# Performance work log

Hardware: AMD Instinct MI355X
Metric: run time of the kernel (lower is better)

## Reference

```python
import jax, jax.numpy as jnp
import numpy as np

N_NODES = 50000
C = 256          # in_channels == hidden_size
E = 800000


def setup_inputs() -> dict:
    key = jax.random.key(0)
    ks = jax.random.split(key, 12)
    x = jax.random.normal(ks[0], (N_NODES, C), dtype=jnp.float32)
    edge_index = jax.random.randint(ks[1], (2, E), 0, N_NODES, dtype=jnp.int64)
    edge_attr = jax.random.uniform(ks[2], (E,), dtype=jnp.float32)
    edge_weights_index = jax.random.randint(ks[3], (2, E), 0, N_NODES, dtype=jnp.int64)
    s = 1.0 / np.sqrt(C)
    # TopKPooling projection vector
    p_pool = jax.random.normal(ks[4], (C,), dtype=jnp.float32) * s
    # GRU (input=C, hidden=C): gates stacked [r, z, n]
    W_ih = jax.random.normal(ks[5], (3 * C, C), dtype=jnp.float32) * s
    W_hh = jax.random.normal(ks[6], (3 * C, C), dtype=jnp.float32) * s
    b_ih = jnp.zeros((3 * C,), dtype=jnp.float32)
    b_hh = jnp.zeros((3 * C,), dtype=jnp.float32)
    # initial evolving GCN weight [C, C]
    W_init = jax.random.normal(ks[7], (C, C), dtype=jnp.float32) * s
    # EdgeDecoder MLP
    lin1_w = jax.random.normal(ks[8], (C, 2 * C), dtype=jnp.float32) / np.sqrt(2 * C)
    lin1_b = jnp.zeros((C,), dtype=jnp.float32)
    lin2_w = jax.random.normal(ks[9], (1, C), dtype=jnp.float32) * s
    lin2_b = jnp.zeros((1,), dtype=jnp.float32)
    return {
        "x": x, "edge_index": edge_index, "edge_attr": edge_attr,
        "edge_weights_index": edge_weights_index,
        "p_pool": p_pool, "W_ih": W_ih, "W_hh": W_hh, "b_ih": b_ih, "b_hh": b_hh,
        "W_init": W_init, "lin1_w": lin1_w, "lin1_b": lin1_b,
        "lin2_w": lin2_w, "lin2_b": lin2_b,
    }


def _forward(x, edge_attr, p_pool, W_ih, W_hh, b_ih, b_hh, W_init,
             lin1_w, lin1_b, lin2_w, lin2_b, edge_index, edge_weights_index):
    n_nodes, c = x.shape
    # --- EvolveGCNH: TopK pooling summary (k = in_channels) ---
    score = x @ p_pool / jnp.linalg.norm(p_pool)          # [N]
    top_score, perm = jax.lax.top_k(score, c)             # [C]
    x_tilde = x[perm] * jnp.tanh(top_score)[:, None]      # [C, C]
    # --- GRU step: input x_tilde (batch=C), hidden = evolving weight W_init ---
    gi = x_tilde @ W_ih.T + b_ih                           # [C, 3C]
    gh = W_init @ W_hh.T + b_hh                            # [C, 3C]
    i_r, i_z, i_n = jnp.split(gi, 3, axis=1)
    h_r, h_z, h_n = jnp.split(gh, 3, axis=1)
    r = jax.nn.sigmoid(i_r + h_r)
    z = jax.nn.sigmoid(i_z + h_z)
    n = jnp.tanh(i_n + r * h_n)
    W = (1.0 - z) * n + z * W_init                         # [C, C] evolved GCN weight
    # --- GCNConv with fixed W, add_self_loops=False ---
    xw = x @ W                                             # [N, C]
    src, dst = edge_index[0], edge_index[1]
    deg = jax.ops.segment_sum(edge_attr, dst, num_segments=n_nodes)
    dinv = jnp.where(deg > 0, jax.lax.rsqrt(jnp.where(deg > 0, deg, 1.0)), 0.0)
    norm = dinv[src] * edge_attr * dinv[dst]               # [E]
    node_emb = jax.ops.segment_sum(xw[src] * norm[:, None], dst,
                                   num_segments=n_nodes)   # [N, C]
    # --- EdgeDecoder: gather src/trg, concat, MLP ---
    s_idx, t_idx = edge_weights_index[0], edge_weights_index[1]
    edge_emb = jnp.concatenate([node_emb[s_idx], node_emb[t_idx]], axis=1)  # [E, 2C]
    h = jax.nn.relu(edge_emb @ lin1_w.T + lin1_b)          # [E, C]
    pred = h @ lin2_w.T + lin2_b                           # [E, 1]
    return pred.reshape(-1)


def reference(x, edge_index, edge_attr, edge_weights_index, p_pool,
              W_ih, W_hh, b_ih, b_hh, W_init, lin1_w, lin1_b, lin2_w, lin2_b):
    # dropout is identity in eval mode
    return _forward(x, edge_attr, p_pool, W_ih, W_hh, b_ih, b_hh, W_init,
                    lin1_w, lin1_b, lin2_w, lin2_b, edge_index, edge_weights_index)
```

## Files before the change

### kernel.cpp

```cpp
#include <hip/hip_runtime.h>
#include <hip/hip_bf16.h>
#include <math.h>


typedef __attribute__((ext_vector_type(8))) short bf16x8;
typedef __attribute__((ext_vector_type(8))) unsigned short u16x8;
typedef __attribute__((ext_vector_type(4))) float f32x4;

#define WSHIFT 9
#define WMASK 511
#define NBUCK 98

__device__ __forceinline__ unsigned f2key(float f) {
  unsigned u = __float_as_uint(f);
  return (u & 0x80000000u) ? ~u : (u | 0x80000000u);
}

__device__ __forceinline__ unsigned short f2bf(float f) {
  unsigned u = __float_as_uint(f);
  unsigned r = u + 0x7fffu + ((u >> 16) & 1u);
  return (unsigned short)(r >> 16);
}
__device__ __forceinline__ float bf2f(unsigned short h) {
  return __uint_as_float((unsigned)h << 16);
}

template <int CTRL>
__device__ __forceinline__ float dpp_add(float s) {
  int t = __builtin_amdgcn_update_dpp(0, __float_as_int(s), CTRL, 0xf, 0xf, false);
  return s + __int_as_float(t);
}

__device__ __forceinline__ void gload16(const void* g, void* l) {
  __builtin_amdgcn_global_load_lds((const __attribute__((address_space(1))) void*)g,
                                   (__attribute__((address_space(3))) void*)l, 16, 0, 0);
}

__global__ __launch_bounds__(256) void init_kernel(const float* __restrict__ lin1,
                                                   unsigned short* __restrict__ WAB,
                                                   int4* __restrict__ zb, int nz4) {
  int b = blockIdx.x, tid = threadIdx.x;
  if (b < 512) {
    int idx = b * 256 + tid;
    int n = idx >> 9, k = idx & 511;
    unsigned short h = f2bf(lin1[idx]);
    if (k < 256)
      WAB[n * 256 + k] = h;
    else
      WAB[(256 + n) * 256 + (k - 256)] = h;
  } else {
    int j = (b - 512) * 256 + tid;
    if (j < nz4) zb[j] = make_int4(0, 0, 0, 0);
  }
}

__global__ __launch_bounds__(256) void score_cast_kernel(const float* __restrict__ x,
                                                         const float* __restrict__ p,
                                                         float* __restrict__ score,
                                                         unsigned short* __restrict__ xh, int N) {
  int node = blockIdx.x * 4 + (threadIdx.x >> 6);
  int lane = threadIdx.x & 63;
  if (node >= N) return;
  float4 xv = ((const float4*)(x + (size_t)node * 256))[lane];
  ushort4 hv;
  hv.x = f2bf(xv.x);
  hv.y = f2bf(xv.y);
  hv.z = f2bf(xv.z);
  hv.w = f2bf(xv.w);
  ((ushort4*)(xh + (size_t)node * 256))[lane] = hv;
  float4 pv = ((const float4*)p)[lane];
  float s = xv.x * pv.x + xv.y * pv.y + xv.z * pv.z + xv.w * pv.w;
  float sp = pv.x * pv.x + pv.y * pv.y + pv.z * pv.z + pv.w * pv.w;
#pragma unroll
  for (int off = 32; off > 0; off >>= 1) {
    s += __shfl_down(s, off, 64);
    sp += __shfl_down(sp, off, 64);
  }
  if (lane == 0) score[node] = s / sqrtf(sp);
}

__global__ __launch_bounds__(256) void hist12_kernel(const float* __restrict__ score, int n,
                                                     int* __restrict__ gh) {
  __shared__ int lh[4096];
  int tid = threadIdx.x;
  for (int i = tid; i < 4096; i += 256) lh[i] = 0;
  __syncthreads();
  int idx = blockIdx.x * 256 + tid;
  int stride = gridDim.x * 256;
  for (int i = idx; i < n; i += stride) {
    unsigned key = f2key(score[i]);
    atomicAdd(&lh[key >> 20], 1);
  }
  __syncthreads();
  for (int i = tid; i < 4096; i += 256) {
    int v = lh[i];
    if (v) atomicAdd(&gh[i], v);
  }
}

__global__ __launch_bounds__(1024) void topk_kernel(const float* __restrict__ score, int n, int k,
                                                    const int* __restrict__ gh,
                                                    int* __restrict__ perm,
                                                    float* __restrict__ tts) {
  __shared__ int part[1024];
  __shared__ unsigned sT;
  int tid = threadIdx.x;
  {
    int b0 = tid * 4;
    int s0 = gh[b0], s1 = gh[b0 + 1], s2 = gh[b0 + 2], s3 = gh[b0 + 3];
    part[tid] = s0 + s1 + s2 + s3;
    __syncthreads();
    for (int off = 1; off < 1024; off <<= 1) {
      int v = part[tid];
      int add = (tid + off < 1024) ? part[tid + off] : 0;
      __syncthreads();
      part[tid] = v + add;
      __syncthreads();
    }
    int sufChunk = part[tid];
    int sufNext = (tid < 1023) ? part[tid + 1] : 0;
    if (sufNext < k && sufChunk >= k) {
      int run = sufNext;
      int b;
      run += s3;
      if (run >= k) b = b0 + 3;
      else {
        run += s2;
        if (run >= k) b = b0 + 2;
        else {
          run += s1;
          b = (run >= k) ? b0 + 1 : b0;
        }
      }
      sT = ((unsigned)b) << 20;
    }
  }
  __syncthreads();
  unsigned T = sT;
  __shared__ unsigned keys[1024];
  __shared__ int idxs[1024];
  __shared__ int cnt;
  if (tid == 0) cnt = 0;
  keys[tid] = 0u;
  idxs[tid] = 0x7fffffff;
  __syncthreads();
  for (int i = tid; i < n; i += 1024) {
    unsigned key = f2key(score[i]);
    if (key >= T) {
      int p = atomicAdd(&cnt, 1);
      if (p < 1024) { keys[p] = key; idxs[p] = i; }
    }
  }
  __syncthreads();
  for (int size = 2; size <= 1024; size <<= 1) {
    for (int stride = size >> 1; stride > 0; stride >>= 1) {
      int j = tid ^ stride;
      if (j > tid) {
        unsigned ka = keys[tid], kb = keys[j];
        int ia = idxs[tid], ib = idxs[j];
        bool aBefore = (ka > kb) || (ka == kb && ia < ib);
        bool up = ((tid & size) == 0);
        if (aBefore != up) {
          keys[tid] = kb; keys[j] = ka;
          idxs[tid] = ib; idxs[j] = ia;
        }
      }
      __syncthreads();
    }
  }
  if (tid < k) {
    int idx = idxs[tid];
    perm[tid] = idx;
    tts[tid] = tanhf(score[idx]);
  }
}

__global__ __launch_bounds__(256) void gru_kernel(const float* __restrict__ x,
                                                  const int* __restrict__ perm,
                                                  const float* __restrict__ tts,
                                                  const float* __restrict__ Wi,
                                                  const float* __restrict__ W_ih,
                                                  const float* __restrict__ W_hh,
                                                  const float* __restrict__ b_ih,
                                                  const float* __restrict__ b_hh,
                                                  unsigned short* __restrict__ WevoT) {
  int i = blockIdx.x, j = threadIdx.x;
  __shared__ float sx[256], sh[256];
  sx[j] = x[(size_t)perm[i] * 256 + j] * tts[i];
  sh[j] = Wi[i * 256 + j];
  __syncthreads();
  float gi[3], gh[3];
#pragma unroll
  for (int g = 0; g < 3; ++g) {
    int row = g * 256 + j;
    const float4* wi4 = (const float4*)(W_ih + (size_t)row * 256);
    const float4* wh4 = (const float4*)(W_hh + (size_t)row * 256);
    float si = 0.f, s2 = 0.f;
    for (int k4 = 0; k4 < 64; ++k4) {
      float4 wv = wi4[k4];
      float4 hv = wh4[k4];
      int k = k4 * 4;
      si += sx[k] * wv.x + sx[k + 1] * wv.y + sx[k + 2] * wv.z + sx[k + 3] * wv.w;
      s2 += sh[k] * hv.x + sh[k + 1] * hv.y + sh[k + 2] * hv.z + sh[k + 3] * hv.w;
    }
    gi[g] = si + b_ih[row];
    gh[g] = s2 + b_hh[row];
  }
  float r = 1.f / (1.f + expf(-(gi[0] + gh[0])));
  float z = 1.f / (1.f + expf(-(gi[1] + gh[1])));
  float nn = tanhf(gi[2] + r * gh[2]);
  float w = (1.f - z) * nn + z * sh[j];
  WevoT[(size_t)j * 256 + i] = f2bf(w);
}

__global__ __launch_bounds__(512) void mfma_gemm128(const unsigned short* __restrict__ A,
                                                    const unsigned short* __restrict__ BT,
                                                    unsigned short* __restrict__ C1,
                                                    unsigned short* __restrict__ C2,
                                                    int M) {
  __shared__ unsigned short sA[128 * 32];
  __shared__ unsigned short sB[256 * 32];
  int tid = threadIdx.x;
  int wave = tid >> 6, lane = tid & 63;
  int quad = lane >> 4, r16 = lane & 15;
  int wm = wave >> 2, wn = wave & 3;
  int mbase = blockIdx.x * 128;
  const unsigned short* Bt = BT + ((size_t)blockIdx.y << 16);
  unsigned short* Cout = blockIdx.y ? C2 : C1;

  int srow = tid >> 2, scolq = tid & 3;
  const unsigned short* gA = A + (size_t)(mbase + srow) * 256 + scolq * 8;
  const unsigned short* gB0 = Bt + (size_t)srow * 256 + scolq * 8;
  const unsigned short* gB1 = Bt + (size_t)(128 + srow) * 256 + scolq * 8;
  unsigned short* lA = sA + wave * 512;
  unsigned short* lB0 = sB + wave * 512;
  unsigned short* lB1 = sB + 4096 + wave * 512;

  f32x4 acc[4][4];
#pragma unroll
  for (int i = 0; i < 4; ++i)
#pragma unroll
    for (int j = 0; j < 4; ++j) acc[i][j] = (f32x4){0.f, 0.f, 0.f, 0.f};

  const unsigned short* pA = sA + (wm * 64 + r16) * 32 + quad * 8;
  const unsigned short* pB = sB + (wn * 64 + r16) * 32 + quad * 8;

  for (int k0 = 0; k0 < 256; k0 += 32) {
    if (k0) __syncthreads();
    gload16(gA + k0, lA);
    gload16(gB0 + k0, lB0);
    gload16(gB1 + k0, lB1);
    __syncthreads();
    bf16x8 af[4], bfr[4];
#pragma unroll
    for (int mt = 0; mt < 4; ++mt) af[mt] = *(const bf16x8*)(pA + mt * 512);
#pragma unroll
    for (int nt = 0; nt < 4; ++nt) bfr[nt] = *(const bf16x8*)(pB + nt * 512);
#pragma unroll
    for (int mt = 0; mt < 4; ++mt)
#pragma unroll
      for (int nt = 0; nt < 4; ++nt)
        acc[mt][nt] = __builtin_amdgcn_mfma_f32_16x16x32_bf16(af[mt], bfr[nt], acc[mt][nt], 0, 0, 0);
  }
#pragma unroll
  for (int mt = 0; mt < 4; ++mt) {
#pragma unroll
    for (int rr = 0; rr < 4; ++rr) {
      int grow = mbase + wm * 64 + mt * 16 + quad * 4 + rr;
      if (grow < M) {
#pragma unroll
        for (int nt = 0; nt < 4; ++nt)
          Cout[(size_t)grow * 256 + wn * 64 + nt * 16 + r16] = f2bf(acc[mt][nt][rr]);
      }
    }
  }
}


__global__ __launch_bounds__(256) void bucket_hist_kernel(const int* __restrict__ ei,
                                                          const int* __restrict__ ewi,
                                                          int* __restrict__ bcnt1,
                                                          int* __restrict__ bcnt2, int E) {
  __shared__ int c1[128], c2[128];
  int tid = threadIdx.x;
  if (tid < 128) { c1[tid] = 0; c2[tid] = 0; }
  __syncthreads();
  int idx = blockIdx.x * 256 + tid;
  int stride = gridDim.x * 256;
  for (int e = idx; e < E; e += stride) {
    atomicAdd(&c1[ei[E + e] >> WSHIFT], 1);
    atomicAdd(&c2[ewi[e] >> WSHIFT], 1);
  }
  __syncthreads();
  if (tid < 128) {
    if (c1[tid]) atomicAdd(&bcnt1[tid], c1[tid]);
    if (c2[tid]) atomicAdd(&bcnt2[tid], c2[tid]);
  }
}

__global__ __launch_bounds__(128) void bucket_scan_kernel(const int* __restrict__ bcnt1,
                                                          const int* __restrict__ bcnt2,
                                                          int* __restrict__ bbase1,
                                                          int* __restrict__ bbase2,
                                                          int* __restrict__ gcur1,
                                                          int* __restrict__ gcur2,
                                                          int* __restrict__ rowp1,
                                                          int* __restrict__ rowp2, int N, int E) {
  __shared__ int ss[128];
  int tid = threadIdx.x;
  int v = (tid < NBUCK) ? bcnt1[tid] : 0;
  ss[tid] = v;
  __syncthreads();
  for (int off = 1; off < 128; off <<= 1) {
    int a = ss[tid];
    int b = (tid >= off) ? ss[tid - off] : 0;
    __syncthreads();
    ss[tid] = a + b;
    __syncthreads();
  }
  int excl = ss[tid] - v;
  if (tid < NBUCK) { bbase1[tid] = excl; gcur1[tid] = excl; }
  if (tid == NBUCK - 1) bbase1[NBUCK] = excl + v;
  __syncthreads();
  v = (tid < NBUCK) ? bcnt2[tid] : 0;
  ss[tid] = v;
  __syncthreads();
  for (int off = 1; off < 128; off <<= 1) {
    int a = ss[tid];
    int b = (tid >= off) ? ss[tid - off] : 0;
    __syncthreads();
    ss[tid] = a + b;
    __syncthreads();
  }
  excl = ss[tid] - v;
  if (tid < NBUCK) { bbase2[tid] = excl; gcur2[tid] = excl; }
  if (tid == NBUCK - 1) bbase2[NBUCK] = excl + v;
  if (tid == 0) { rowp1[N] = E; rowp2[N] = E; }
}

__global__ __launch_bounds__(256) void p1_both_kernel(const int* __restrict__ ei,
                                                      const float* __restrict__ attr,
                                                      int* __restrict__ gcur1,
                                                      int2* __restrict__ stage1,
                                                      const int* __restrict__ ewi,
                                                      int* __restrict__ gcur2,
                                                      int2* __restrict__ stage2,
                                                      int E, int nb) {
  __shared__ int cnt[128], cur[128];
  int tid = threadIdx.x;
  bool conv = blockIdx.x < nb;
  int base = (conv ? blockIdx.x : blockIdx.x - nb) * 4096;
  int* gcur = conv ? gcur1 : gcur2;
  int2* stage = conv ? stage1 : stage2;
  if (tid < 128) cnt[tid] = 0;
  __syncthreads();
  int bk[16];
  int2 pl[16];
#pragma unroll
  for (int i = 0; i < 16; ++i) {
    int e = base + i * 256 + tid;
    bk[i] = -1;
    if (e < E) {
      if (conv) {
        int d = ei[E + e];
        int s = ei[e];
        bk[i] = d >> WSHIFT;
        pl[i] = make_int2(s | ((d & WMASK) << 16), __float_as_int(attr[e]));
      } else {
        int s = ewi[e];
        int d = ewi[E + e];
        bk[i] = s >> WSHIFT;
        pl[i] = make_int2(d | ((s & WMASK) << 16), e);
      }
      atomicAdd(&cnt[bk[i]], 1);
    }
  }
  __syncthreads();
  if (tid < NBUCK) {
    int c = cnt[tid];
    cur[tid] = c ? atomicAdd(&gcur[tid], c) : 0;
  }
  __syncthreads();
#pragma unroll
  for (int i = 0; i < 16; ++i) {
    if (bk[i] >= 0) {
      int pos = atomicAdd(&cur[bk[i]], 1);
      stage[pos] = pl[i];
    }
  }
}

__global__ __launch_bounds__(256) void p2_kernel(const int2* __restrict__ stage1,
                                                 const int* __restrict__ bbase1,
                                                 int2* __restrict__ esv,
                                                 int* __restrict__ rowp1,
                                                 float* __restrict__ dinv,
                                                 const int2* __restrict__ stage2,
                                                 const int* __restrict__ bbase2,
                                                 int2* __restrict__ eto,
                                                 int* __restrict__ rowp2, int N) {
  __shared__ int cnt[512];
  __shared__ float degs[512];
  __shared__ int pref[512];
  __shared__ int ss[256];
  int tid = threadIdx.x;
  bool isConv = blockIdx.x < NBUCK;
  int b = isConv ? blockIdx.x : blockIdx.x - NBUCK;
  const int2* stage = isConv ? stage1 : stage2;
  const int* bbase = isConv ? bbase1 : bbase2;
  int beg = bbase[b], end = bbase[b + 1];
  int node0 = b << WSHIFT;
  cnt[tid] = 0; cnt[tid + 256] = 0;
  degs[tid] = 0.f; degs[tid + 256] = 0.f;
  __syncthreads();
  for (int j = beg + tid; j < end; j += 256) {
    int2 p = stage[j];
    int loc = p.x >> 16;
    atomicAdd(&cnt[loc], 1);
    if (isConv) atomicAdd(&degs[loc], __int_as_float(p.y));
  }
  __syncthreads();
  int c0 = cnt[2 * tid], c1 = cnt[2 * tid + 1];
  ss[tid] = c0 + c1;
  __syncthreads();
  for (int off = 1; off < 256; off <<= 1) {
    int a = ss[tid];
    int bb = (tid >= off) ? ss[tid - off] : 0;
    __syncthreads();
    ss[tid] = a + bb;
    __syncthreads();
  }
  int excl = (tid ? ss[tid - 1] : 0);
  pref[2 * tid] = excl;
  pref[2 * tid + 1] = excl + c0;
  __syncthreads();
#pragma unroll
  for (int h = 0; h < 2; ++h) {
    int i = tid + h * 256;
    int node = node0 + i;
    if (node < N) {
      if (isConv) {
        rowp1[node] = beg + pref[i];
        float d = degs[i];
        dinv[node] = d > 0.f ? 1.f / sqrtf(d) : 0.f;
      } else {
        rowp2[node] = beg + pref[i];
      }
    }
  }
  __syncthreads();
  int2* outb = isConv ? esv : eto;
  for (int j = beg + tid; j < end; j += 256) {
    int2 p = stage[j];
    int loc = p.x >> 16;
    int pos = beg + atomicAdd(&pref[loc], 1);
    outb[pos] = make_int2(p.x & 0xFFFF, p.y);
  }
}

__global__ __launch_bounds__(256) void gcn_gather(const unsigned short* __restrict__ xw,
                                                  const int* __restrict__ row_ptr,
                                                  const int2* __restrict__ esv,
                                                  const float* __restrict__ dinv,
                                                  unsigned short* __restrict__ ne, int N) {
  int node = blockIdx.x * 4 + (threadIdx.x >> 6);
  int lane = threadIdx.x & 63;
  int g = lane & 15, q = lane >> 4;
  if (node >= N) return;
  int beg = row_ptr[node], end = row_ptr[node + 1];
  float acc[16];
#pragma unroll
  for (int c = 0; c < 16; ++c) acc[c] = 0.f;
  const unsigned short* xb = xw + g * 16;

  for (int cb = beg; cb < end; cb += 64) {
    int cend = cb + 64 < end ? cb + 64 : end;
    int me = cb + lane;
    int2 mm = (me < cend) ? esv[me] : make_int2(0, 0);
    int mx = mm.x;
    float mv = __int_as_float(mm.y) * dinv[mx];

    float vA = 0.f, vB = 0.f, vC = 0.f;
    u16x8 rAa, rAb, rBa, rBb, rCa, rCb;
    {
      int e = cb + q;
      int sx = __shfl(mx, q, 64);
      float tv = __shfl(mv, q, 64);
      vA = (e < cend) ? tv : 0.f;
      rAa = *(const u16x8*)(xb + (size_t)sx * 256);
      rAb = *(const u16x8*)(xb + (size_t)sx * 256 + 8);
    }
    if (cb + 4 < cend) {
      int e = cb + 4 + q;
      int sx = __shfl(mx, 4 + q, 64);
      float tv = __shfl(mv, 4 + q, 64);
      vB = (e < cend) ? tv : 0.f;
      rBa = *(const u16x8*)(xb + (size_t)sx * 256);
      rBb = *(const u16x8*)(xb + (size_t)sx * 256 + 8);
    } else { rBa = rAa; rBb = rAb; }
    if (cb + 8 < cend) {
      int e = cb + 8 + q;
      int sx = __shfl(mx, 8 + q, 64);
      float tv = __shfl(mv, 8 + q, 64);
      vC = (e < cend) ? tv : 0.f;
      rCa = *(const u16x8*)(xb + (size_t)sx * 256);
      rCb = *(const u16x8*)(xb + (size_t)sx * 256 + 8);
    } else { rCa = rAa; rCb = rAb; }

    for (int jb = cb; jb < cend; jb += 12) {
#pragma unroll
      for (int c = 0; c < 8; ++c) acc[c] += bf2f(rAa[c]) * vA;
#pragma unroll
      for (int c = 0; c < 8; ++c) acc[8 + c] += bf2f(rAb[c]) * vA;
      vA = 0.f;
      if (jb + 12 < cend) {
        int e = jb + 12 + q;
        int idx = (e - cb) & 63;
        int sx = __shfl(mx, idx, 64);
        float tv = __shfl(mv, idx, 64);
        vA = (e < cend) ? tv : 0.f;
        rAa = *(const u16x8*)(xb + (size_t)sx * 256);
        rAb = *(const u16x8*)(xb + (size_t)sx * 256 + 8);
      }
#pragma unroll
      for (int c = 0; c < 8; ++c) acc[c] += bf2f(rBa[c]) * vB;
#pragma unroll
      for (int c = 0; c < 8; ++c) acc[8 + c] += bf2f(rBb[c]) * vB;
      vB = 0.f;
      if (jb + 16 < cend) {
        int e = jb + 16 + q;
        int idx = (e - cb) & 63;
        int sx = __shfl(mx, idx, 64);
        float tv = __shfl(mv, idx, 64);
        vB = (e < cend) ? tv : 0.f;
        rBa = *(const u16x8*)(xb + (size_t)sx * 256);
        rBb = *(const u16x8*)(xb + (size_t)sx * 256 + 8);
      }
#pragma unroll
      for (int c = 0; c < 8; ++c) acc[c] += bf2f(rCa[c]) * vC;
#pragma unroll
      for (int c = 0; c < 8; ++c) acc[8 + c] += bf2f(rCb[c]) * vC;
      vC = 0.f;
      if (jb + 20 < cend) {
        int e = jb + 20 + q;
        int idx = (e - cb) & 63;
        int sx = __shfl(mx, idx, 64);
        float tv = __shfl(mv, idx, 64);
        vC = (e < cend) ? tv : 0.f;
        rCa = *(const u16x8*)(xb + (size_t)sx * 256);
        rCb = *(const u16x8*)(xb + (size_t)sx * 256 + 8);
      }
    }
  }
#pragma unroll
  for (int c = 0; c < 16; ++c) {
    acc[c] += __shfl_xor(acc[c], 16, 64);
    acc[c] += __shfl_xor(acc[c], 32, 64);
  }
  if (q == 0) {
    float dd = dinv[node];
    u16x8 o0, o1;
#pragma unroll
    for (int c = 0; c < 8; ++c) {
      o0[c] = f2bf(acc[c] * dd);
      o1[c] = f2bf(acc[8 + c] * dd);
    }
    *(u16x8*)(ne + (size_t)node * 256 + g * 16) = o0;
    *(u16x8*)(ne + (size_t)node * 256 + g * 16 + 8) = o1;
  }
}

__global__ __launch_bounds__(256) void edge_decode_csr(const unsigned short* __restrict__ A,
                                                       const unsigned short* __restrict__ Bm,
                                                       const int* __restrict__ row_ptr,
                                                       const int2* __restrict__ eto,
                                                       const float* __restrict__ b1,
                                                       const float* __restrict__ w2,
                                                       const float* __restrict__ b2,
                                                       float* __restrict__ out, int N) {
  int node = blockIdx.x * 4 + (threadIdx.x >> 6);
  int lane = threadIdx.x & 63;
  int g = lane & 15, q = lane >> 4;
  if (node >= N) return;
  int beg = row_ptr[node], end = row_ptr[node + 1];
  if (beg >= end) return;
  float a[16], w[16];
  {
    u16x8 a0 = *(const u16x8*)(A + (size_t)node * 256 + g * 16);
    u16x8 a1 = *(const u16x8*)(A + (size_t)node * 256 + g * 16 + 8);
    const float4* bp = (const float4*)(b1 + g * 16);
    const float4* wp = (const float4*)(w2 + g * 16);
#pragma unroll
    for (int i = 0; i < 4; ++i) {
      float4 bv = bp[i];
      float4 wv = wp[i];
      a[i * 4 + 0] = (i < 2 ? bf2f(a0[i * 4 + 0]) : bf2f(a1[i * 4 - 8])) + bv.x;
      a[i * 4 + 1] = (i < 2 ? bf2f(a0[i * 4 + 1]) : bf2f(a1[i * 4 - 7])) + bv.y;
      a[i * 4 + 2] = (i < 2 ? bf2f(a0[i * 4 + 2]) : bf2f(a1[i * 4 - 6])) + bv.z;
      a[i * 4 + 3] = (i < 2 ? bf2f(a0[i * 4 + 3]) : bf2f(a1[i * 4 - 5])) + bv.w;
      w[i * 4 + 0] = wv.x;
      w[i * 4 + 1] = wv.y;
      w[i * 4 + 2] = wv.z;
      w[i * 4 + 3] = wv.w;
    }
  }
  float base = b2[0];
  const unsigned short* Bb = Bm + g * 16;

  for (int cb = beg; cb < end; cb += 64) {
    int cend = cb + 64 < end ? cb + 64 : end;
    int me = cb + lane;
    int2 mm = (me < cend) ? eto[me] : make_int2(0, 0);
    int mx = mm.x, my = mm.y;

    bool okA = false, okB = false, okC = false;
    int oA = 0, oB = 0, oC = 0;
    u16x8 rAa, rAb, rBa, rBb, rCa, rCb;
    {
      int e = cb + q;
      int sx = __shfl(mx, q, 64);
      oA = __shfl(my, q, 64);
      okA = e < cend;
      rAa = *(const u16x8*)(Bb + (size_t)sx * 256);
      rAb = *(const u16x8*)(Bb + (size_t)sx * 256 + 8);
    }
    if (cb + 4 < cend) {
      int e = cb + 4 + q;
      int sx = __shfl(mx, 4 + q, 64);
      oB = __shfl(my, 4 + q, 64);
      okB = e < cend;
      rBa = *(const u16x8*)(Bb + (size_t)sx * 256);
      rBb = *(const u16x8*)(Bb + (size_t)sx * 256 + 8);
    } else { rBa = rAa; rBb = rAb; }
    if (cb + 8 < cend) {
      int e = cb + 8 + q;
      int sx = __shfl(mx, 8 + q, 64);
      oC = __shfl(my, 8 + q, 64);
      okC = e < cend;
      rCa = *(const u16x8*)(Bb + (size_t)sx * 256);
      rCb = *(const u16x8*)(Bb + (size_t)sx * 256 + 8);
    } else { rCa = rAa; rCb = rAb; }

    for (int jb = cb; jb < cend; jb += 12) {
      {
        float s0 = 0.f, s1 = 0.f;
#pragma unroll
        for (int c = 0; c < 8; ++c) s0 += fmaxf(a[c] + bf2f(rAa[c]), 0.f) * w[c];
#pragma unroll
        for (int c = 0; c < 8; ++c) s1 += fmaxf(a[8 + c] + bf2f(rAb[c]), 0.f) * w[8 + c];
        float s = s0 + s1;
        s = dpp_add<0x128>(s);
        s = dpp_add<0x124>(s);
        s = dpp_add<0x122>(s);
        s = dpp_add<0x121>(s);
        if (g == 0 && okA) out[oA] = s + base;
      }
      okA = false;
      if (jb + 12 < cend) {
        int e = jb + 12 + q;
        int idx = (e - cb) & 63;
        int sx = __shfl(mx, idx, 64);
        oA = __shfl(my, idx, 64);
        okA = e < cend;
        rAa = *(const u16x8*)(Bb + (size_t)sx * 256);
        rAb = *(const u16x8*)(Bb + (size_t)sx * 256 + 8);
      }
      {
        float s0 = 0.f, s1 = 0.f;
#pragma unroll
        for (int c = 0; c < 8; ++c) s0 += fmaxf(a[c] + bf2f(rBa[c]), 0.f) * w[c];
#pragma unroll
        for (int c = 0; c < 8; ++c) s1 += fmaxf(a[8 + c] + bf2f(rBb[c]), 0.f) * w[8 + c];
        float s = s0 + s1;
        s = dpp_add<0x128>(s);
        s = dpp_add<0x124>(s);
        s = dpp_add<0x122>(s);
        s = dpp_add<0x121>(s);
        if (g == 0 && okB) out[oB] = s + base;
      }
      okB = false;
      if (jb + 16 < cend) {
        int e = jb + 16 + q;
        int idx = (e - cb) & 63;
        int sx = __shfl(mx, idx, 64);
        oB = __shfl(my, idx, 64);
        okB = e < cend;
        rBa = *(const u16x8*)(Bb + (size_t)sx * 256);
        rBb = *(const u16x8*)(Bb + (size_t)sx * 256 + 8);
      }
      {
        float s0 = 0.f, s1 = 0.f;
#pragma unroll
        for (int c = 0; c < 8; ++c) s0 += fmaxf(a[c] + bf2f(rCa[c]), 0.f) * w[c];
#pragma unroll
        for (int c = 0; c < 8; ++c) s1 += fmaxf(a[8 + c] + bf2f(rCb[c]), 0.f) * w[8 + c];
        float s = s0 + s1;
        s = dpp_add<0x128>(s);
        s = dpp_add<0x124>(s);
        s = dpp_add<0x122>(s);
        s = dpp_add<0x121>(s);
        if (g == 0 && okC) out[oC] = s + base;
      }
      okC = false;
      if (jb + 20 < cend) {
        int e = jb + 20 + q;
        int idx = (e - cb) & 63;
        int sx = __shfl(mx, idx, 64);
        oC = __shfl(my, idx, 64);
        okC = e < cend;
        rCa = *(const u16x8*)(Bb + (size_t)sx * 256);
        rCb = *(const u16x8*)(Bb + (size_t)sx * 256 + 8);
      }
    }
  }
}

extern "C" void kernel_launch(void* const* d_in, const int* in_sizes, int n_in,
                              void* d_out, int out_size, void* d_ws, size_t ws_size,
                              hipStream_t stream) {
  const float* x      = (const float*)d_in[0];
  const int*   ei     = (const int*)d_in[1];
  const float* attr   = (const float*)d_in[2];
  const int*   ewi    = (const int*)d_in[3];
  const float* p_pool = (const float*)d_in[4];
  const float* W_ih   = (const float*)d_in[5];
  const float* W_hh   = (const float*)d_in[6];
  const float* b_ih   = (const float*)d_in[7];
  const float* b_hh   = (const float*)d_in[8];
  const float* W_init = (const float*)d_in[9];
  const float* lin1_w = (const float*)d_in[10];
  const float* lin1_b = (const float*)d_in[11];
  const float* lin2_w = (const float*)d_in[12];
  const float* lin2_b = (const float*)d_in[13];
  float* out = (float*)d_out;

  const int C = 256;
  const int N = in_sizes[0] / C;
  const int E = in_sizes[2];

  char* ws = (char*)d_ws;
  size_t off = 0;
  auto alloc = [&](size_t bytes) {
    size_t o = off;
    off = (off + bytes + 255) & ~(size_t)255;
    return o;
  };
  float*          score  = (float*)(ws + alloc((size_t)N * 4));
  int*            perm   = (int*)(ws + alloc(C * 4));
  float*          tts    = (float*)(ws + alloc(C * 4));
  unsigned short* WevoT  = (unsigned short*)(ws + alloc((size_t)C * C * 2));
  unsigned short* WAB    = (unsigned short*)(ws + alloc((size_t)2 * C * C * 2));
  int   zeroInts = 4096 + 128 + 128;
  char* zbase    = ws + alloc((size_t)zeroInts * 4);
  int* ghist = (int*)zbase;
  int* bcnt1 = (int*)(zbase + 4096 * 4);
  int* bcnt2 = (int*)(zbase + 4096 * 4 + 128 * 4);
  int*            bbase1 = (int*)(ws + alloc((NBUCK + 1) * 4));
  int*            bbase2 = (int*)(ws + alloc((NBUCK + 1) * 4));
  int*            gcur1  = (int*)(ws + alloc(128 * 4));
  int*            gcur2  = (int*)(ws + alloc(128 * 4));
  float*          dinv   = (float*)(ws + alloc((size_t)N * 4));
  int*            rowp1  = (int*)(ws + alloc((size_t)(N + 1) * 4));
  int*            rowp2  = (int*)(ws + alloc((size_t)(N + 1) * 4));
  int2*           stage1 = (int2*)(ws + alloc((size_t)E * 8));
  int2*           stage2 = (int2*)(ws + alloc((size_t)E * 8));
  int2*           esv    = (int2*)(ws + alloc((size_t)E * 8));
  int2*           eto    = (int2*)(ws + alloc((size_t)E * 8));
  unsigned short* xh     = (unsigned short*)(ws + alloc((size_t)N * C * 2));
  unsigned short* xwh    = (unsigned short*)(ws + alloc((size_t)N * C * 2));
  unsigned short* Bbf    = (unsigned short*)(ws + alloc((size_t)N * C * 2));
  unsigned short* ne  = xh;
  unsigned short* Abf = xwh;

  int nz4 = (zeroInts + 3) / 4;
  int nbP1 = (E + 4095) / 4096;

  init_kernel<<<512 + (nz4 + 255) / 256, 256, 0, stream>>>(lin1_w, WAB, (int4*)zbase, nz4);

  score_cast_kernel<<<(N + 3) / 4, 256, 0, stream>>>(x, p_pool, score, xh, N);

  hist12_kernel<<<64, 256, 0, stream>>>(score, N, ghist);
  topk_kernel<<<1, 1024, 0, stream>>>(score, N, C, ghist, perm, tts);

  gru_kernel<<<C, C, 0, stream>>>(x, perm, tts, W_init, W_ih, W_hh, b_ih, b_hh, WevoT);

  mfma_gemm128<<<dim3((N + 127) / 128, 1), 512, 0, stream>>>(xh, WevoT, xwh, xwh, N);

  bucket_hist_kernel<<<256, 256, 0, stream>>>(ei, ewi, bcnt1, bcnt2, E);
  bucket_scan_kernel<<<1, 128, 0, stream>>>(bcnt1, bcnt2, bbase1, bbase2, gcur1, gcur2,
                                            rowp1, rowp2, N, E);
  p1_both_kernel<<<2 * nbP1, 256, 0, stream>>>(ei, attr, gcur1, stage1,
                                               ewi, gcur2, stage2, E, nbP1);
  p2_kernel<<<2 * NBUCK, 256, 0, stream>>>(stage1, bbase1, esv, rowp1, dinv,
                                           stage2, bbase2, eto, rowp2, N);

  gcn_gather<<<(N + 3) / 4, 256, 0, stream>>>(xwh, rowp1, esv, dinv, ne, N);

  mfma_gemm128<<<dim3((N + 127) / 128, 2), 512, 0, stream>>>(ne, WAB, Abf, Bbf, N);

  edge_decode_csr<<<(N + 3) / 4, 256, 0, stream>>>(Abf, Bbf, rowp2, eto,
                                                   lin1_b, lin2_w, lin2_b, out, N);
}
```

Baseline: 454.9 us.

## Merge independent topk/GRU and edge-bucketing stages into shared kernel launches

```diff
diff --git a/kernel.cpp b/kernel.cpp
--- a/kernel.cpp
+++ b/kernel.cpp
@@ -54,163 +54,351 @@
   }
 }
 
-__global__ __launch_bounds__(256) void score_cast_kernel(const float* __restrict__ x,
-                                                         const float* __restrict__ p,
-                                                         float* __restrict__ score,
-                                                         unsigned short* __restrict__ xh, int N) {
-  int node = blockIdx.x * 4 + (threadIdx.x >> 6);
-  int lane = threadIdx.x & 63;
-  if (node >= N) return;
-  float4 xv = ((const float4*)(x + (size_t)node * 256))[lane];
-  ushort4 hv;
-  hv.x = f2bf(xv.x);
-  hv.y = f2bf(xv.y);
-  hv.z = f2bf(xv.z);
-  hv.w = f2bf(xv.w);
-  ((ushort4*)(xh + (size_t)node * 256))[lane] = hv;
-  float4 pv = ((const float4*)p)[lane];
-  float s = xv.x * pv.x + xv.y * pv.y + xv.z * pv.z + xv.w * pv.w;
-  float sp = pv.x * pv.x + pv.y * pv.y + pv.z * pv.z + pv.w * pv.w;
-#pragma unroll
-  for (int off = 32; off > 0; off >>= 1) {
-    s += __shfl_down(s, off, 64);
-    sp += __shfl_down(sp, off, 64);
-  }
-  if (lane == 0) score[node] = s / sqrtf(sp);
-}
-
-__global__ __launch_bounds__(256) void hist12_kernel(const float* __restrict__ score, int n,
-                                                     int* __restrict__ gh) {
-  __shared__ int lh[4096];
+__global__ __launch_bounds__(256) void fusedA_kernel(const float* __restrict__ x,
+                                                     const float* __restrict__ p,
+                                                     float* __restrict__ score,
+                                                     unsigned short* __restrict__ xh, int N,
+                                                     const int* __restrict__ ei,
+                                                     const int* __restrict__ ewi,
+                                                     int* __restrict__ bcnt1,
+                                                     int* __restrict__ bcnt2, int E) {
   int tid = threadIdx.x;
-  for (int i = tid; i < 4096; i += 256) lh[i] = 0;
-  __syncthreads();
-  int idx = blockIdx.x * 256 + tid;
-  int stride = gridDim.x * 256;
-  for (int i = idx; i < n; i += stride) {
-    unsigned key = f2key(score[i]);
-    atomicAdd(&lh[key >> 20], 1);
-  }
-  __syncthreads();
-  for (int i = tid; i < 4096; i += 256) {
-    int v = lh[i];
-    if (v) atomicAdd(&gh[i], v);
-  }
-}
-
-__global__ __launch_bounds__(1024) void topk_kernel(const float* __restrict__ score, int n, int k,
-                                                    const int* __restrict__ gh,
-                                                    int* __restrict__ perm,
-                                                    float* __restrict__ tts) {
-  __shared__ int part[1024];
-  __shared__ unsigned sT;
+  if (blockIdx.x < 256) {
+    __shared__ int c1[128], c2[128];
+    if (tid < 128) { c1[tid] = 0; c2[tid] = 0; }
+    __syncthreads();
+    int idx = blockIdx.x * 256 + tid;
+    int stride = 256 * 256;
+    for (int e = idx; e < E; e += stride) {
+      atomicAdd(&c1[ei[E + e] >> WSHIFT], 1);
+      atomicAdd(&c2[ewi[e] >> WSHIFT], 1);
+    }
+    __syncthreads();
+    if (tid < 128) {
+      if (c1[tid]) atomicAdd(&bcnt1[tid], c1[tid]);
+      if (c2[tid]) atomicAdd(&bcnt2[tid], c2[tid]);
+    }
+  } else {
+    int node = (blockIdx.x - 256) * 4 + (tid >> 6);
+    int lane = tid & 63;
+    if (node >= N) return;
+    float4 xv = ((const float4*)(x + (size_t)node * 256))[lane];
+    ushort4 hv;
+    hv.x = f2bf(xv.x);
+    hv.y = f2bf(xv.y);
+    hv.z = f2bf(xv.z);
+    hv.w = f2bf(xv.w);
+    ((ushort4*)(xh + (size_t)node * 256))[lane] = hv;
+    float4 pv = ((const float4*)p)[lane];
+    float s = xv.x * pv.x + xv.y * pv.y + xv.z * pv.z + xv.w * pv.w;
+    float sp = pv.x * pv.x + pv.y * pv.y + pv.z * pv.z + pv.w * pv.w;
+#pragma unroll
+    for (int off = 32; off > 0; off >>= 1) {
+      s += __shfl_down(s, off, 64);
+      sp += __shfl_down(sp, off, 64);
+    }
+    if (lane == 0) score[node] = s / sqrtf(sp);
+  }
+}
+
+__global__ __launch_bounds__(256) void fusedB_kernel(const float* __restrict__ score, int n,
+                                                     int* __restrict__ gh,
+                                                     const int* __restrict__ bcnt1,
+                                                     const int* __restrict__ bcnt2,
+                                                     int* __restrict__ bbase1,
+                                                     int* __restrict__ bbase2,
+                                                     int* __restrict__ gcur1,
+                                                     int* __restrict__ gcur2,
+                                                     int* __restrict__ rowp1,
+                                                     int* __restrict__ rowp2, int N, int E) {
   int tid = threadIdx.x;
-  {
-    int b0 = tid * 4;
-    int s0 = gh[b0], s1 = gh[b0 + 1], s2 = gh[b0 + 2], s3 = gh[b0 + 3];
-    part[tid] = s0 + s1 + s2 + s3;
-    __syncthreads();
-    for (int off = 1; off < 1024; off <<= 1) {
-      int v = part[tid];
-      int add = (tid + off < 1024) ? part[tid + off] : 0;
+  if (blockIdx.x < 64) {
+    __shared__ int lh[4096];
+    for (int i = tid; i < 4096; i += 256) lh[i] = 0;
+    __syncthreads();
+    int idx = blockIdx.x * 256 + tid;
+    int stride = 64 * 256;
+    for (int i = idx; i < n; i += stride) {
+      unsigned key = f2key(score[i]);
+      atomicAdd(&lh[key >> 20], 1);
+    }
+    __syncthreads();
+    for (int i = tid; i < 4096; i += 256) {
+      int v = lh[i];
+      if (v) atomicAdd(&gh[i], v);
+    }
+  } else {
+    __shared__ int ss[128];
+    int v = 0;
+    if (tid < 128) { v = (tid < NBUCK) ? bcnt1[tid] : 0; ss[tid] = v; }
+    __syncthreads();
+    for (int off = 1; off < 128; off <<= 1) {
+      int a = 0, b = 0;
+      if (tid < 128) { a = ss[tid]; b = (tid >= off) ? ss[tid - off] : 0; }
       __syncthreads();
-      part[tid] = v + add;
+      if (tid < 128) ss[tid] = a + b;
       __syncthreads();
     }
-    int sufChunk = part[tid];
-    int sufNext = (tid < 1023) ? part[tid + 1] : 0;
-    if (sufNext < k && sufChunk >= k) {
-      int run = sufNext;
-      int b;
-      run += s3;
-      if (run >= k) b = b0 + 3;
-      else {
-        run += s2;
-        if (run >= k) b = b0 + 2;
+    if (tid < 128) {
+      int excl = ss[tid] - v;
+      if (tid < NBUCK) { bbase1[tid] = excl; gcur1[tid] = excl; }
+      if (tid == NBUCK - 1) bbase1[NBUCK] = excl + v;
+    }
+    __syncthreads();
+    int v2 = 0;
+    if (tid < 128) { v2 = (tid < NBUCK) ? bcnt2[tid] : 0; ss[tid] = v2; }
+    __syncthreads();
+    for (int off = 1; off < 128; off <<= 1) {
+      int a = 0, b = 0;
+      if (tid < 128) { a = ss[tid]; b = (tid >= off) ? ss[tid - off] : 0; }
+      __syncthreads();
+      if (tid < 128) ss[tid] = a + b;
+      __syncthreads();
+    }
+    if (tid < 128) {
+      int excl = ss[tid] - v2;
+      if (tid < NBUCK) { bbase2[tid] = excl; gcur2[tid] = excl; }
+      if (tid == NBUCK - 1) bbase2[NBUCK] = excl + v2;
+    }
+    if (tid == 0) { rowp1[N] = E; rowp2[N] = E; }
+  }
+}
+
+__global__ __launch_bounds__(1024) void fusedC_kernel(const int* __restrict__ ei,
+                                                      const float* __restrict__ attr,
+                                                      int* __restrict__ gcur1,
+                                                      int2* __restrict__ stage1,
+                                                      const int* __restrict__ ewi,
+                                                      int* __restrict__ gcur2,
+                                                      int2* __restrict__ stage2,
+                                                      int E, int nb,
+                                                      const float* __restrict__ score, int n, int k,
+                                                      const int* __restrict__ gh,
+                                                      int* __restrict__ perm,
+                                                      float* __restrict__ tts) {
+  int tid = threadIdx.x;
+  if ((int)blockIdx.x < 2 * nb) {
+    bool conv = (int)blockIdx.x < nb;
+    __shared__ int pcnt[128], pcur[128];
+    int base = (conv ? blockIdx.x : blockIdx.x - nb) * 8192;
+    int* gcur = conv ? gcur1 : gcur2;
+    int2* stage = conv ? stage1 : stage2;
+    if (tid < 128) pcnt[tid] = 0;
+    __syncthreads();
+    int bk[8];
+    int2 pl[8];
+#pragma unroll
+    for (int i = 0; i < 8; ++i) {
+      int e = base + i * 1024 + tid;
+      bk[i] = -1;
+      if (e < E) {
+        if (conv) {
+          int d = ei[E + e];
+          int s = ei[e];
+          bk[i] = d >> WSHIFT;
+          pl[i] = make_int2(s | ((d & WMASK) << 16), __float_as_int(attr[e]));
+        } else {
+          int s = ewi[e];
+          int d = ewi[E + e];
+          bk[i] = s >> WSHIFT;
+          pl[i] = make_int2(d | ((s & WMASK) << 16), e);
+        }
+        atomicAdd(&pcnt[bk[i]], 1);
+      }
+    }
+    __syncthreads();
+    if (tid < NBUCK) {
+      int c = pcnt[tid];
+      pcur[tid] = c ? atomicAdd(&gcur[tid], c) : 0;
+    }
+    __syncthreads();
+#pragma unroll
+    for (int i = 0; i < 8; ++i) {
+      if (bk[i] >= 0) {
+        int pos = atomicAdd(&pcur[bk[i]], 1);
+        stage[pos] = pl[i];
+      }
+    }
+  } else {
+    __shared__ int part[1024];
+    __shared__ unsigned sT;
+    {
+      int b0 = tid * 4;
+      int s0 = gh[b0], s1 = gh[b0 + 1], s2 = gh[b0 + 2], s3 = gh[b0 + 3];
+      part[tid] = s0 + s1 + s2 + s3;
+      __syncthreads();
+      for (int off = 1; off < 1024; off <<= 1) {
+        int v = part[tid];
+        int add = (tid + off < 1024) ? part[tid + off] : 0;
+        __syncthreads();
+        part[tid] = v + add;
+        __syncthreads();
+      }
+      int sufChunk = part[tid];
+      int sufNext = (tid < 1023) ? part[tid + 1] : 0;
+      if (sufNext < k && sufChunk >= k) {
+        int run = sufNext;
+        int b;
+        run += s3;
+        if (run >= k) b = b0 + 3;
         else {
-          run += s1;
-          b = (run >= k) ? b0 + 1 : b0;
+          run += s2;
+          if (run >= k) b = b0 + 2;
+          else {
+            run += s1;
+            b = (run >= k) ? b0 + 1 : b0;
+          }
         }
-      }
-      sT = ((unsigned)b) << 20;
-    }
-  }
-  __syncthreads();
-  unsigned T = sT;
-  __shared__ unsigned keys[1024];
-  __shared__ int idxs[1024];
-  __shared__ int cnt;
-  if (tid == 0) cnt = 0;
-  keys[tid] = 0u;
-  idxs[tid] = 0x7fffffff;
-  __syncthreads();
-  for (int i = tid; i < n; i += 1024) {
-    unsigned key = f2key(score[i]);
-    if (key >= T) {
-      int p = atomicAdd(&cnt, 1);
-      if (p < 1024) { keys[p] = key; idxs[p] = i; }
-    }
-  }
-  __syncthreads();
-  for (int size = 2; size <= 1024; size <<= 1) {
-    for (int stride = size >> 1; stride > 0; stride >>= 1) {
-      int j = tid ^ stride;
-      if (j > tid) {
-        unsigned ka = keys[tid], kb = keys[j];
-        int ia = idxs[tid], ib = idxs[j];
-        bool aBefore = (ka > kb) || (ka == kb && ia < ib);
-        bool up = ((tid & size) == 0);
-        if (aBefore != up) {
-          keys[tid] = kb; keys[j] = ka;
-          idxs[tid] = ib; idxs[j] = ia;
+        sT = ((unsigned)b) << 20;
+      }
+    }
+    __syncthreads();
+    unsigned T = sT;
+    __shared__ unsigned keys[1024];
+    __shared__ int idxs[1024];
+    __shared__ int cnt;
+    if (tid == 0) cnt = 0;
+    keys[tid] = 0u;
+    idxs[tid] = 0x7fffffff;
+    __syncthreads();
+    for (int i = tid; i < n; i += 1024) {
+      unsigned key = f2key(score[i]);
+      if (key >= T) {
+        int p = atomicAdd(&cnt, 1);
+        if (p < 1024) { keys[p] = key; idxs[p] = i; }
+      }
+    }
+    __syncthreads();
+    for (int size = 2; size <= 1024; size <<= 1) {
+      for (int stride = size >> 1; stride > 0; stride >>= 1) {
+        int j = tid ^ stride;
+        if (j > tid) {
+          unsigned ka = keys[tid], kb = keys[j];
+          int ia = idxs[tid], ib = idxs[j];
+          bool aBefore = (ka > kb) || (ka == kb && ia < ib);
+          bool up = ((tid & size) == 0);
+          if (aBefore != up) {
+            keys[tid] = kb; keys[j] = ka;
+            idxs[tid] = ib; idxs[j] = ia;
+          }
         }
-      }
+        __syncthreads();
+      }
+    }
+    if (tid < k) {
+      int idx = idxs[tid];
+      perm[tid] = idx;
+      tts[tid] = tanhf(score[idx]);
+    }
+  }
+}
+
+__global__ __launch_bounds__(256) void fusedD_kernel(const float* __restrict__ x,
+                                                     const int* __restrict__ perm,
+                                                     const float* __restrict__ tts,
+                                                     const float* __restrict__ Wi,
+                                                     const float* __restrict__ W_ih,
+                                                     const float* __restrict__ W_hh,
+                                                     const float* __restrict__ b_ih,
+                                                     const float* __restrict__ b_hh,
+                                                     unsigned short* __restrict__ WevoT,
+                                                     const int2* __restrict__ stage1,
+                                                     const int* __restrict__ bbase1,
+                                                     int2* __restrict__ esv,
+                                                     int* __restrict__ rowp1,
+                                                     float* __restrict__ dinv,
+                                                     const int2* __restrict__ stage2,
+                                                     const int* __restrict__ bbase2,
+                                                     int2* __restrict__ eto,
+                                                     int* __restrict__ rowp2, int N) {
+  int tid = threadIdx.x;
+  if (blockIdx.x < 256) {
+    int i = blockIdx.x, j = tid;
+    __shared__ float sx[256], sh[256];
+    sx[j] = x[(size_t)perm[i] * 256 + j] * tts[i];
+    sh[j] = Wi[i * 256 + j];
+    __syncthreads();
+    float gi[3], gh[3];
+#pragma unroll
+    for (int g = 0; g < 3; ++g) {
+      int row = g * 256 + j;
+      const float4* wi4 = (const float4*)(W_ih + (size_t)row * 256);
+      const float4* wh4 = (const float4*)(W_hh + (size_t)row * 256);
+      float si = 0.f, s2 = 0.f;
+      for (int k4 = 0; k4 < 64; ++k4) {
+        float4 wv = wi4[k4];
+        float4 hv = wh4[k4];
+        int k = k4 * 4;
+        si += sx[k] * wv.x + sx[k + 1] * wv.y + sx[k + 2] * wv.z + sx[k + 3] * wv.w;
+        s2 += sh[k] * hv.x + sh[k + 1] * hv.y + sh[k + 2] * hv.z + sh[k + 3] * hv.w;
+      }
+      gi[g] = si + b_ih[row];
+      gh[g] = s2 + b_hh[row];
+    }
+    float r = 1.f / (1.f + expf(-(gi[0] + gh[0])));
+    float z = 1.f / (1.f + expf(-(gi[1] + gh[1])));
+    float nn = tanhf(gi[2] + r * gh[2]);
+    float w = (1.f - z) * nn + z * sh[j];
+    WevoT[(size_t)j * 256 + i] = f2bf(w);
+  } else {
+    __shared__ int cnt[512];
+    __shared__ float degs[512];
+    __shared__ int pref[512];
+    __shared__ int ss[256];
+    int bb2 = blockIdx.x - 256;
+    bool isConv = bb2 < NBUCK;
+    int b = isConv ? bb2 : bb2 - NBUCK;
+    const int2* stage = isConv ? stage1 : stage2;
+    const int* bbase = isConv ? bbase1 : bbase2;
+    int beg = bbase[b], end = bbase[b + 1];
+    int node0 = b << WSHIFT;
+    cnt[tid] = 0; cnt[tid + 256] = 0;
+    degs[tid] = 0.f; degs[tid + 256] = 0.f;
+    __syncthreads();
+    for (int j = beg + tid; j < end; j += 256) {
+      int2 p = stage[j];
+      int loc = p.x >> 16;
+      atomicAdd(&cnt[loc], 1);
+      if (isConv) atomicAdd(&degs[loc], __int_as_float(p.y));
+    }
+    __syncthreads();
+    int c0 = cnt[2 * tid], c1 = cnt[2 * tid + 1];
+    ss[tid] = c0 + c1;
+    __syncthreads();
+    for (int off = 1; off < 256; off <<= 1) {
+      int a = ss[tid];
+      int bsum = (tid >= off) ? ss[tid - off] : 0;
       __syncthreads();
-    }
-  }
-  if (tid < k) {
-    int idx = idxs[tid];
-    perm[tid] = idx;
-    tts[tid] = tanhf(score[idx]);
-  }
-}
-
-__global__ __launch_bounds__(256) void gru_kernel(const float* __restrict__ x,
-                                                  const int* __restrict__ perm,
-                                                  const float* __restrict__ tts,
-                                                  const float* __restrict__ Wi,
-                                                  const float* __restrict__ W_ih,
-                                                  const float* __restrict__ W_hh,
-                                                  const float* __restrict__ b_ih,
-                                                  const float* __restrict__ b_hh,
-                                                  unsigned short* __restrict__ WevoT) {
-  int i = blockIdx.x, j = threadIdx.x;
-  __shared__ float sx[256], sh[256];
-  sx[j] = x[(size_t)perm[i] * 256 + j] * tts[i];
-  sh[j] = Wi[i * 256 + j];
-  __syncthreads();
-  float gi[3], gh[3];
-#pragma unroll
-  for (int g = 0; g < 3; ++g) {
-    int row = g * 256 + j;
-    const float4* wi4 = (const float4*)(W_ih + (size_t)row * 256);
-    const float4* wh4 = (const float4*)(W_hh + (size_t)row * 256);
-    float si = 0.f, s2 = 0.f;
-    for (int k4 = 0; k4 < 64; ++k4) {
-      float4 wv = wi4[k4];
-      float4 hv = wh4[k4];
-      int k = k4 * 4;
-      si += sx[k] * wv.x + sx[k + 1] * wv.y + sx[k + 2] * wv.z + sx[k + 3] * wv.w;
-      s2 += sh[k] * hv.x + sh[k + 1] * hv.y + sh[k + 2] * hv.z + sh[k + 3] * hv.w;
-    }
-    gi[g] = si + b_ih[row];
-    gh[g] = s2 + b_hh[row];
-  }
-  float r = 1.f / (1.f + expf(-(gi[0] + gh[0])));
-  float z = 1.f / (1.f + expf(-(gi[1] + gh[1])));
-  float nn = tanhf(gi[2] + r * gh[2]);
-  float w = (1.f - z) * nn + z * sh[j];
-  WevoT[(size_t)j * 256 + i] = f2bf(w);
+      ss[tid] = a + bsum;
+      __syncthreads();
+    }
+    int excl = (tid ? ss[tid - 1] : 0);
+    pref[2 * tid] = excl;
+    pref[2 * tid + 1] = excl + c0;
+    __syncthreads();
+#pragma unroll
+    for (int h = 0; h < 2; ++h) {
+      int i = tid + h * 256;
+      int node = node0 + i;
+      if (node < N) {
+        if (isConv) {
+          rowp1[node] = beg + pref[i];
+          float d = degs[i];
+          dinv[node] = d > 0.f ? 1.f / sqrtf(d) : 0.f;
+        } else {
+          rowp2[node] = beg + pref[i];
+        }
+      }
+    }
+    __syncthreads();
+    int2* outb = isConv ? esv : eto;
+    for (int j = beg + tid; j < end; j += 256) {
+      int2 p = stage[j];
+      int loc = p.x >> 16;
+      int pos = beg + atomicAdd(&pref[loc], 1);
+      outb[pos] = make_int2(p.x & 0xFFFF, p.y);
+    }
+  }
 }
 
 __global__ __launch_bounds__(512) void mfma_gemm128(const unsigned short* __restrict__ A,
@@ -273,188 +461,6 @@
           Cout[(size_t)grow * 256 + wn * 64 + nt * 16 + r16] = f2bf(acc[mt][nt][rr]);
       }
     }
-  }
-}
-
-
-__global__ __launch_bounds__(256) void bucket_hist_kernel(const int* __restrict__ ei,
-                                                          const int* __restrict__ ewi,
-                                                          int* __restrict__ bcnt1,
-                                                          int* __restrict__ bcnt2, int E) {
-  __shared__ int c1[128], c2[128];
-  int tid = threadIdx.x;
-  if (tid < 128) { c1[tid] = 0; c2[tid] = 0; }
-  __syncthreads();
-  int idx = blockIdx.x * 256 + tid;
-  int stride = gridDim.x * 256;
-  for (int e = idx; e < E; e += stride) {
-    atomicAdd(&c1[ei[E + e] >> WSHIFT], 1);
-    atomicAdd(&c2[ewi[e] >> WSHIFT], 1);
-  }
-  __syncthreads();
-  if (tid < 128) {
-    if (c1[tid]) atomicAdd(&bcnt1[tid], c1[tid]);
-    if (c2[tid]) atomicAdd(&bcnt2[tid], c2[tid]);
-  }
-}
-
-__global__ __launch_bounds__(128) void bucket_scan_kernel(const int* __restrict__ bcnt1,
-                                                          const int* __restrict__ bcnt2,
-                                                          int* __restrict__ bbase1,
-                                                          int* __restrict__ bbase2,
-                                                          int* __restrict__ gcur1,
-                                                          int* __restrict__ gcur2,
-                                                          int* __restrict__ rowp1,
-                                                          int* __restrict__ rowp2, int N, int E) {
-  __shared__ int ss[128];
-  int tid = threadIdx.x;
-  int v = (tid < NBUCK) ? bcnt1[tid] : 0;
-  ss[tid] = v;
-  __syncthreads();
-  for (int off = 1; off < 128; off <<= 1) {
-    int a = ss[tid];
-    int b = (tid >= off) ? ss[tid - off] : 0;
-    __syncthreads();
-    ss[tid] = a + b;
-    __syncthreads();
-  }
-  int excl = ss[tid] - v;
-  if (tid < NBUCK) { bbase1[tid] = excl; gcur1[tid] = excl; }
-  if (tid == NBUCK - 1) bbase1[NBUCK] = excl + v;
-  __syncthreads();
-  v = (tid < NBUCK) ? bcnt2[tid] : 0;
-  ss[tid] = v;
-  __syncthreads();
-  for (int off = 1; off < 128; off <<= 1) {
-    int a = ss[tid];
-    int b = (tid >= off) ? ss[tid - off] : 0;
-    __syncthreads();
-    ss[tid] = a + b;
-    __syncthreads();
-  }
-  excl = ss[tid] - v;
-  if (tid < NBUCK) { bbase2[tid] = excl; gcur2[tid] = excl; }
-  if (tid == NBUCK - 1) bbase2[NBUCK] = excl + v;
-  if (tid == 0) { rowp1[N] = E; rowp2[N] = E; }
-}
-
-__global__ __launch_bounds__(256) void p1_both_kernel(const int* __restrict__ ei,
-                                                      const float* __restrict__ attr,
-                                                      int* __restrict__ gcur1,
-                                                      int2* __restrict__ stage1,
-                                                      const int* __restrict__ ewi,
-                                                      int* __restrict__ gcur2,
-                                                      int2* __restrict__ stage2,
-                                                      int E, int nb) {
-  __shared__ int cnt[128], cur[128];
-  int tid = threadIdx.x;
-  bool conv = blockIdx.x < nb;
-  int base = (conv ? blockIdx.x : blockIdx.x - nb) * 4096;
-  int* gcur = conv ? gcur1 : gcur2;
-  int2* stage = conv ? stage1 : stage2;
-  if (tid < 128) cnt[tid] = 0;
-  __syncthreads();
-  int bk[16];
-  int2 pl[16];
-#pragma unroll
-  for (int i = 0; i < 16; ++i) {
-    int e = base + i * 256 + tid;
-    bk[i] = -1;
-    if (e < E) {
-      if (conv) {
-        int d = ei[E + e];
-        int s = ei[e];
-        bk[i] = d >> WSHIFT;
-        pl[i] = make_int2(s | ((d & WMASK) << 16), __float_as_int(attr[e]));
-      } else {
-        int s = ewi[e];
-        int d = ewi[E + e];
-        bk[i] = s >> WSHIFT;
-        pl[i] = make_int2(d | ((s & WMASK) << 16), e);
-      }
-      atomicAdd(&cnt[bk[i]], 1);
-    }
-  }
-  __syncthreads();
-  if (tid < NBUCK) {
-    int c = cnt[tid];
-    cur[tid] = c ? atomicAdd(&gcur[tid], c) : 0;
-  }
-  __syncthreads();
-#pragma unroll
-  for (int i = 0; i < 16; ++i) {
-    if (bk[i] >= 0) {
-      int pos = atomicAdd(&cur[bk[i]], 1);
-      stage[pos] = pl[i];
-    }
-  }
-}
-
-__global__ __launch_bounds__(256) void p2_kernel(const int2* __restrict__ stage1,
-                                                 const int* __restrict__ bbase1,
-                                                 int2* __restrict__ esv,
-                                                 int* __restrict__ rowp1,
-                                                 float* __restrict__ dinv,
-                                                 const int2* __restrict__ stage2,
-                                                 const int* __restrict__ bbase2,
-                                                 int2* __restrict__ eto,
-                                                 int* __restrict__ rowp2, int N) {
-  __shared__ int cnt[512];
-  __shared__ float degs[512];
-  __shared__ int pref[512];
-  __shared__ int ss[256];
-  int tid = threadIdx.x;
-  bool isConv = blockIdx.x < NBUCK;
-  int b = isConv ? blockIdx.x : blockIdx.x - NBUCK;
-  const int2* stage = isConv ? stage1 : stage2;
-  const int* bbase = isConv ? bbase1 : bbase2;
-  int beg = bbase[b], end = bbase[b + 1];
-  int node0 = b << WSHIFT;
-  cnt[tid] = 0; cnt[tid + 256] = 0;
-  degs[tid] = 0.f; degs[tid + 256] = 0.f;
-  __syncthreads();
-  for (int j = beg + tid; j < end; j += 256) {
-    int2 p = stage[j];
-    int loc = p.x >> 16;
-    atomicAdd(&cnt[loc], 1);
-    if (isConv) atomicAdd(&degs[loc], __int_as_float(p.y));
-  }
-  __syncthreads();
-  int c0 = cnt[2 * tid], c1 = cnt[2 * tid + 1];
-  ss[tid] = c0 + c1;
-  __syncthreads();
-  for (int off = 1; off < 256; off <<= 1) {
-    int a = ss[tid];
-    int bb = (tid >= off) ? ss[tid - off] : 0;
-    __syncthreads();
-    ss[tid] = a + bb;
-    __syncthreads();
-  }
-  int excl = (tid ? ss[tid - 1] : 0);
-  pref[2 * tid] = excl;
-  pref[2 * tid + 1] = excl + c0;
-  __syncthreads();
-#pragma unroll
-  for (int h = 0; h < 2; ++h) {
-    int i = tid + h * 256;
-    int node = node0 + i;
-    if (node < N) {
-      if (isConv) {
-        rowp1[node] = beg + pref[i];
-        float d = degs[i];
-        dinv[node] = d > 0.f ? 1.f / sqrtf(d) : 0.f;
-      } else {
-        rowp2[node] = beg + pref[i];
-      }
-    }
-  }
-  __syncthreads();
-  int2* outb = isConv ? esv : eto;
-  for (int j = beg + tid; j < end; j += 256) {
-    int2 p = stage[j];
-    int loc = p.x >> 16;
-    int pos = beg + atomicAdd(&pref[loc], 1);
-    outb[pos] = make_int2(p.x & 0xFFFF, p.y);
   }
 }
 
@@ -773,26 +779,27 @@
   unsigned short* Abf = xwh;
 
   int nz4 = (zeroInts + 3) / 4;
-  int nbP1 = (E + 4095) / 4096;
+  int nbP1 = (E + 8191) / 8192;
 
   init_kernel<<<512 + (nz4 + 255) / 256, 256, 0, stream>>>(lin1_w, WAB, (int4*)zbase, nz4);
 
-  score_cast_kernel<<<(N + 3) / 4, 256, 0, stream>>>(x, p_pool, score, xh, N);
-
-  hist12_kernel<<<64, 256, 0, stream>>>(score, N, ghist);
-  topk_kernel<<<1, 1024, 0, stream>>>(score, N, C, ghist, perm, tts);
-
-  gru_kernel<<<C, C, 0, stream>>>(x, perm, tts, W_init, W_ih, W_hh, b_ih, b_hh, WevoT);
+  fusedA_kernel<<<256 + (N + 3) / 4, 256, 0, stream>>>(x, p_pool, score, xh, N,
+                                                       ei, ewi, bcnt1, bcnt2, E);
+
+  fusedB_kernel<<<65, 256, 0, stream>>>(score, N, ghist, bcnt1, bcnt2,
+                                        bbase1, bbase2, gcur1, gcur2,
+                                        rowp1, rowp2, N, E);
+
+  fusedC_kernel<<<2 * nbP1 + 1, 1024, 0, stream>>>(ei, attr, gcur1, stage1,
+                                                   ewi, gcur2, stage2, E, nbP1,
+                                                   score, N, C, ghist, perm, tts);
+
+  fusedD_kernel<<<256 + 2 * NBUCK, 256, 0, stream>>>(x, perm, tts, W_init,
+                                                     W_ih, W_hh, b_ih, b_hh, WevoT,
+                                                     stage1, bbase1, esv, rowp1, dinv,
+                                                     stage2, bbase2, eto, rowp2, N);
 
   mfma_gemm128<<<dim3((N + 127) / 128, 1), 512, 0, stream>>>(xh, WevoT, xwh, xwh, N);
-
-  bucket_hist_kernel<<<256, 256, 0, stream>>>(ei, ewi, bcnt1, bcnt2, E);
-  bucket_scan_kernel<<<1, 128, 0, stream>>>(bcnt1, bcnt2, bbase1, bbase2, gcur1, gcur2,
-                                            rowp1, rowp2, N, E);
-  p1_both_kernel<<<2 * nbP1, 256, 0, stream>>>(ei, attr, gcur1, stage1,
-                                               ewi, gcur2, stage2, E, nbP1);
-  p2_kernel<<<2 * NBUCK, 256, 0, stream>>>(stage1, bbase1, esv, rowp1, dinv,
-                                           stage2, bbase2, eto, rowp2, N);
 
   gcn_gather<<<(N + 3) / 4, 256, 0, stream>>>(xwh, rowp1, esv, dinv, ne, N);
 
```

After: 405.6 us. 10.8% less time.
